# Kernel tuning notes

Measured on AMD Instinct MI355X. Metric: run time of the kernel, lower is better.

## Reference

```python
import jax, jax.numpy as jnp
import numpy as np

N_SEGMENT = 16
N_HEADS = 12
DIM = 768
HEAD_DIM = DIM // N_HEADS
LN_EPS = 1e-5


def setup_inputs() -> dict:
    key = jax.random.key(0)
    ks = jax.random.split(key, 12)
    nt, p, c = 512, 197, DIM
    s = 1.0 / np.sqrt(c)
    return {
        "x": jax.random.normal(ks[0], (nt, p, c), dtype=jnp.float32),
        "w1": jax.random.uniform(ks[1], (1, 1, c), dtype=jnp.float32) * 2.0 - 1.0,
        "ln_g": jnp.ones((c,), dtype=jnp.float32),
        "ln_b": jnp.zeros((c,), dtype=jnp.float32),
        "Wq": jax.random.normal(ks[2], (c, c), dtype=jnp.float32) * s,
        "bq": jax.random.normal(ks[3], (c,), dtype=jnp.float32) * 0.02,
        "Wk": jax.random.normal(ks[4], (c, c), dtype=jnp.float32) * s,
        "bk": jax.random.normal(ks[5], (c,), dtype=jnp.float32) * 0.02,
        "Wv": jax.random.normal(ks[6], (c, c), dtype=jnp.float32) * s,
        "bv": jax.random.normal(ks[7], (c,), dtype=jnp.float32) * 0.02,
        "Wo": jax.random.normal(ks[8], (c, c), dtype=jnp.float32) * s,
        "bo": jax.random.normal(ks[9], (c,), dtype=jnp.float32) * 0.02,
    }


def _layer_norm(x, g, b):
    mu = jnp.mean(x, axis=-1, keepdims=True)
    var = jnp.mean(jnp.square(x - mu), axis=-1, keepdims=True)
    return (x - mu) * jax.lax.rsqrt(var + LN_EPS) * g + b


def _attention(h, Wq, bq, Wk, bk, Wv, bv, Wo, bo):
    # h: [B, T, C]
    B, T, C = h.shape
    def heads(y):
        return y.reshape(B, T, N_HEADS, HEAD_DIM).transpose(0, 2, 1, 3)
    q = heads(h @ Wq + bq)  # [B, H, T, Dh]
    k = heads(h @ Wk + bk)
    v = heads(h @ Wv + bv)
    scores = jnp.einsum("bhtd,bhsd->bhts", q, k) / jnp.sqrt(jnp.float32(HEAD_DIM))
    probs = jax.nn.softmax(scores, axis=-1)
    ctx = jnp.einsum("bhts,bhsd->bhtd", probs, v)
    ctx = ctx.transpose(0, 2, 1, 3).reshape(B, T, C)
    return ctx @ Wo + bo


def reference(x, w1, ln_g, ln_b, Wq, bq, Wk, bk, Wv, bv, Wo, bo):
    nt, p, c = x.shape
    B = nt // N_SEGMENT
    xr = x.reshape(B, N_SEGMENT, p, c)
    s = xr[:, :, 0]  # CLS tokens [B, T, C]
    # weighted temporal shift (in torch this mutates the view; residual sees it)
    s_shift = s.at[:, 1:].add(s[:, :-1] * w1)
    t = _layer_norm(s_shift, ln_g, ln_b)
    t = _attention(t, Wq, bq, Wk, bk, Wv, bv, Wo, bo)
    t = t + s_shift  # residual uses SHIFTED tokens (aliasing in torch source)
    out = xr.at[:, :, 0].set(t)
    return out.reshape(nt, p, c)
```

## Files before the change

### kernel.cpp

```cpp
#include <hip/hip_runtime.h>
#include <math.h>

typedef __attribute__((ext_vector_type(8))) short short8;
typedef __attribute__((ext_vector_type(4))) float f32x4;
typedef __attribute__((ext_vector_type(4))) unsigned short us4;

constexpr int NSEG = 16;
constexpr int CC   = 768;
constexpr int PP   = 197;
constexpr int NH   = 12;
constexpr int HD   = 64;
constexpr int NT   = 512;
constexpr int MN   = NT * CC;
constexpr float LN_EPS = 1e-5f;

constexpr unsigned CPT  = 196 * CC / 4;
constexpr unsigned ROW4 = CC / 4;
constexpr unsigned W4TOT = (unsigned)NT * CPT;

constexpr unsigned L1 = 7077888u;
constexpr unsigned L2 = 5406720u;
constexpr unsigned L3 = 4423680u;
constexpr unsigned L4 = W4TOT - L1 - L2 - L3;
constexpr unsigned B2 = L1, B3 = L1 + L2, B4 = L1 + L2 + L3;

__device__ inline unsigned short f2bf(float f) {
    unsigned u = __float_as_uint(f);
    u += 0x7fffu + ((u >> 16) & 1u);
    return (unsigned short)(u >> 16);
}
__device__ inline float bf2f(unsigned short v) {
    return __uint_as_float((unsigned)v << 16);
}
__device__ inline unsigned cidx(unsigned i) {
    unsigned t = i / CPT;
    return i + t * ROW4 + ROW4;
}
__device__ inline void copy_strided(const float* __restrict__ xf, float* __restrict__ of,
                                    unsigned base, unsigned len,
                                    unsigned ct, unsigned nth) {
    const f32x4* __restrict__ x4 = (const f32x4*)xf;
    f32x4* __restrict__ o4 = (f32x4*)of;
    for (unsigned i = ct; i < len; i += nth) {
        unsigned a = cidx(base + i);
        f32x4 v = __builtin_nontemporal_load(x4 + a);
        o4[a] = v;
    }
}

template<bool ADD_RES, bool BF16_OUT>
__device__ inline void gemm_tile(const unsigned short* __restrict__ A,
                                 const unsigned short* __restrict__ Bt,
                                 const float* __restrict__ bias,
                                 const float* __restrict__ res,
                                 float* __restrict__ outf, unsigned short* __restrict__ outb,
                                 int by, int bx, size_t orow) {
    int tid  = threadIdx.x;
    int lane = tid & 63, wv = tid >> 6;
    int wr = wv >> 1, wc = wv & 1;
    int l15 = lane & 15, lh = lane >> 4;
    int m0 = by * 64 + wr * 32;
    int n0 = bx * 64 + wc * 32;
    f32x4 acc[2][2] = {};
    const unsigned short* Ar0 = A  + (size_t)(m0 + l15) * CC + lh * 8;
    const unsigned short* Ar1 = Ar0 + 16 * CC;
    const unsigned short* Br0 = Bt + (size_t)(n0 + l15) * CC + lh * 8;
    const unsigned short* Br1 = Br0 + 16 * CC;
    #pragma unroll 4
    for (int k0 = 0; k0 < CC; k0 += 32) {
        short8 a0 = *(const short8*)(Ar0 + k0);
        short8 a1 = *(const short8*)(Ar1 + k0);
        short8 b0 = *(const short8*)(Br0 + k0);
        short8 b1 = *(const short8*)(Br1 + k0);
        acc[0][0] = __builtin_amdgcn_mfma_f32_16x16x32_bf16(a0, b0, acc[0][0], 0, 0, 0);
        acc[0][1] = __builtin_amdgcn_mfma_f32_16x16x32_bf16(a0, b1, acc[0][1], 0, 0, 0);
        acc[1][0] = __builtin_amdgcn_mfma_f32_16x16x32_bf16(a1, b0, acc[1][0], 0, 0, 0);
        acc[1][1] = __builtin_amdgcn_mfma_f32_16x16x32_bf16(a1, b1, acc[1][1], 0, 0, 0);
    }
    #pragma unroll
    for (int mf = 0; mf < 2; ++mf)
        #pragma unroll
        for (int nf = 0; nf < 2; ++nf)
            #pragma unroll
            for (int r = 0; r < 4; ++r) {
                int row = m0 + mf * 16 + lh * 4 + r;
                int col = n0 + nf * 16 + l15;
                float v = acc[mf][nf][r] + bias[col];
                if (ADD_RES) v += res[(size_t)row * CC + col];
                if (BF16_OUT) outb[(size_t)row * orow + col] = f2bf(v);
                else          outf[(size_t)row * orow + col] = v;
            }
}

__global__ __launch_bounds__(256) void k1(const float* __restrict__ x, const float* __restrict__ w1,
        const float* __restrict__ g, const float* __restrict__ bln,
        const float* __restrict__ Wq, const float* __restrict__ Wk,
        const float* __restrict__ Wv, const float* __restrict__ Wo,
        float* __restrict__ s_shift, unsigned short* __restrict__ tln,
        unsigned short* __restrict__ wt, float* __restrict__ out) {
    __shared__ float smem[32 * 33];
    int bid = blockIdx.x, tid = threadIdx.x;
    if (bid < 288) {
        #pragma unroll
        for (int rep = 0; rep < 8; ++rep) {
            int idx = bid + rep * 288;
            int mat = idx / 576, tile = idx % 576;
            int tr = tile / 24, tc = tile % 24;
            const float* W = mat == 0 ? Wq : mat == 1 ? Wk : mat == 2 ? Wv : Wo;
            int lr = tid >> 3, lc = (tid & 7) * 4;
            float4 v = *(const float4*)(W + (size_t)(tr * 32 + lr) * CC + tc * 32 + lc);
            smem[lr * 33 + lc + 0] = v.x; smem[lr * 33 + lc + 1] = v.y;
            smem[lr * 33 + lc + 2] = v.z; smem[lr * 33 + lc + 3] = v.w;
            __syncthreads();
            int ln_ = tid >> 3, kc = (tid & 7) * 4;
            us4 o;
            #pragma unroll
            for (int j = 0; j < 4; ++j) o[j] = f2bf(smem[(kc + j) * 33 + ln_]);
            *(us4*)(wt + (size_t)mat * CC * CC + (size_t)(tc * 32 + ln_) * CC + tr * 32 + kc) = o;
            __syncthreads();
        }
    } else if (bid < 288 + NT) {
        int r = bid - 288, seg = r & (NSEG - 1);
        float vals[3]; float local = 0.f;
        #pragma unroll
        for (int i = 0; i < 3; ++i) {
            int c = tid + i * 256;
            float v = x[(size_t)r * PP * CC + c];
            if (seg > 0) v += w1[c] * x[(size_t)(r - 1) * PP * CC + c];
            vals[i] = v; local += v;
        }
        smem[tid] = local; __syncthreads();
        for (int off = 128; off > 0; off >>= 1) {
            if (tid < off) smem[tid] += smem[tid + off];
            __syncthreads();
        }
        float mu = smem[0] * (1.0f / CC); __syncthreads();
        float lv = 0.f;
        #pragma unroll
        for (int i = 0; i < 3; ++i) { float d = vals[i] - mu; lv += d * d; }
        smem[tid] = lv; __syncthreads();
        for (int off = 128; off > 0; off >>= 1) {
            if (tid < off) smem[tid] += smem[tid + off];
            __syncthreads();
        }
        float rstd = rsqrtf(smem[0] * (1.0f / CC) + LN_EPS);
        #pragma unroll
        for (int i = 0; i < 3; ++i) {
            int c = tid + i * 256;
            s_shift[(size_t)r * CC + c] = vals[i];
            tln[(size_t)r * CC + c] = f2bf((vals[i] - mu) * rstd * g[c] + bln[c]);
        }
    }
    copy_strided(x, out, 0u, L1, (unsigned)bid * 256 + tid, 2048u * 256);
}

__global__ __launch_bounds__(256) void k2(const unsigned short* __restrict__ tln,
        const unsigned short* __restrict__ wt,
        const float* __restrict__ bq, const float* __restrict__ bk, const float* __restrict__ bv,
        unsigned short* __restrict__ qkvb,
        const float* __restrict__ x, float* __restrict__ out) {
    int bid = blockIdx.x, tid = threadIdx.x;
    if (bid < 288) {
        int z = bid / 96, rem = bid % 96;
        int by = rem / 12, bx = rem % 12;
        const float* bias = z == 0 ? bq : (z == 1 ? bk : bv);
        gemm_tile<false, true>(tln, wt + (size_t)z * CC * CC, bias, nullptr,
                               nullptr, qkvb + (size_t)z * MN, by, bx, CC);
    } else {
        copy_strided(x, out, B2, L2, (unsigned)(bid - 288) * 256 + tid, 1760u * 256);
    }
}

__global__ __launch_bounds__(256) void k3(const unsigned short* __restrict__ qkvb,
        unsigned short* __restrict__ ctxb,
        const float* __restrict__ x, float* __restrict__ out) {
    int bid = blockIdx.x, tid = threadIdx.x;
    if (bid < 384) {
        const unsigned short* qb = qkvb;
        const unsigned short* kb = qkvb + MN;
        const unsigned short* vb = qkvb + 2 * MN;
        int bb = bid / NH, h = bid % NH;
        __shared__ float qs[16][HD], ks[16][HD], vs[16][HD];
        __shared__ float sc[16][17];
        __shared__ float rsum[16];
        for (int i = tid; i < 16 * HD; i += 256) {
            int t = i >> 6, d = i & 63;
            size_t gidx = (size_t)(bb * NSEG + t) * CC + h * HD + d;
            qs[t][d] = bf2f(qb[gidx]); ks[t][d] = bf2f(kb[gidx]); vs[t][d] = bf2f(vb[gidx]);
        }
        __syncthreads();
        {
            int t = tid >> 4, s = tid & 15;
            float acc = 0.f;
            #pragma unroll
            for (int d = 0; d < HD; ++d) acc += qs[t][d] * ks[s][d];
            sc[t][s] = acc * 0.125f;
        }
        __syncthreads();
        if (tid < 16) {
            float m = -1e30f;
            #pragma unroll
            for (int s = 0; s < 16; ++s) m = fmaxf(m, sc[tid][s]);
            float sum = 0.f;
            #pragma unroll
            for (int s = 0; s < 16; ++s) { float e = __expf(sc[tid][s] - m); sc[tid][s] = e; sum += e; }
            rsum[tid] = sum;
        }
        __syncthreads();
        for (int i = tid; i < 16 * HD; i += 256) {
            int t = i >> 6, d = i & 63;
            float acc = 0.f;
            #pragma unroll
            for (int s = 0; s < 16; ++s) acc += sc[t][s] * vs[s][d];
            ctxb[(size_t)(bb * NSEG + t) * CC + h * HD + d] = f2bf(acc / rsum[t]);
        }
    } else {
        copy_strided(x, out, B3, L3, (unsigned)(bid - 384) * 256 + tid, 1664u * 256);
    }
}

__global__ __launch_bounds__(256) void k4(const unsigned short* __restrict__ ctxb,
        const unsigned short* __restrict__ wto,
        const float* __restrict__ bo, const float* __restrict__ s_shift,
        float* __restrict__ out, const float* __restrict__ x) {
    int bid = blockIdx.x, tid = threadIdx.x;
    if (bid < 96) {
        int by = bid / 12, bx = bid % 12;
        gemm_tile<true, false>(ctxb, wto, bo, s_shift, out, nullptr, by, bx, (size_t)PP * CC);
    } else {
        copy_strided(x, out, B4, L4, (unsigned)(bid - 96) * 256 + tid, 1952u * 256);
    }
}

extern "C" void kernel_launch(void* const* d_in, const int* in_sizes, int n_in,
                              void* d_out, int out_size, void* d_ws, size_t ws_size,
                              hipStream_t stream) {
    const float* x    = (const float*)d_in[0];
    const float* w1   = (const float*)d_in[1];
    const float* ln_g = (const float*)d_in[2];
    const float* ln_b = (const float*)d_in[3];
    const float* Wq   = (const float*)d_in[4];
    const float* bq   = (const float*)d_in[5];
    const float* Wk   = (const float*)d_in[6];
    const float* bk   = (const float*)d_in[7];
    const float* Wv   = (const float*)d_in[8];
    const float* bv   = (const float*)d_in[9];
    const float* Wo   = (const float*)d_in[10];
    const float* bo   = (const float*)d_in[11];
    float* out = (float*)d_out;

    float* s_shift = (float*)d_ws;
    unsigned short* tln  = (unsigned short*)(s_shift + MN);
    unsigned short* qkvb = tln + MN;
    unsigned short* ctxb = qkvb + 3 * (size_t)MN;
    unsigned short* wt   = ctxb + MN;

    k1<<<2048, 256, 0, stream>>>(x, w1, ln_g, ln_b, Wq, Wk, Wv, Wo, s_shift, tln, wt, out);
    k2<<<2048, 256, 0, stream>>>(tln, wt, bq, bk, bv, qkvb, x, out);
    k3<<<2048, 256, 0, stream>>>(qkvb, ctxb, x, out);
    k4<<<2048, 256, 0, stream>>>(ctxb, wt + (size_t)3 * CC * CC, bo, s_shift, out, x);
}
```

Before: 142.2 us.

## Fuse output projection into attention kernel with per-head atomic accumulation

Removes the fourth kernel: each attention block keeps its per-head context in LDS and multiplies it by the matching 64-row slice of Wo with MFMA. It then atomically adds the partial products into the CLS rows of the output. Eight extra blocks in the QKV kernel first write the residual plus bias (s_shift + bo) into those rows, so the atomics accumulate on top of them. This drops one launch and the ctx round-trip through global memory, and the bulk copy is spread across three kernels instead of four. The cost is a 12-way float atomic contention per output element and a non-deterministic summation order.

Result: slower. 153.8 us (+8.2%).

```diff
diff --git a/kernel.cpp b/kernel.cpp
--- a/kernel.cpp
+++ b/kernel.cpp
@@ -18,11 +18,10 @@
 constexpr unsigned ROW4 = CC / 4;
 constexpr unsigned W4TOT = (unsigned)NT * CPT;
 
-constexpr unsigned L1 = 7077888u;
-constexpr unsigned L2 = 5406720u;
-constexpr unsigned L3 = 4423680u;
-constexpr unsigned L4 = W4TOT - L1 - L2 - L3;
-constexpr unsigned B2 = L1, B3 = L1 + L2, B4 = L1 + L2 + L3;
+constexpr unsigned L1 = 7340032u;
+constexpr unsigned L2 = 6291456u;
+constexpr unsigned L3 = W4TOT - L1 - L2;
+constexpr unsigned B2 = L1, B3 = L1 + L2;
 
 __device__ inline unsigned short f2bf(float f) {
     unsigned u = __float_as_uint(f);
@@ -48,13 +47,11 @@
     }
 }
 
-template<bool ADD_RES, bool BF16_OUT>
-__device__ inline void gemm_tile(const unsigned short* __restrict__ A,
-                                 const unsigned short* __restrict__ Bt,
-                                 const float* __restrict__ bias,
-                                 const float* __restrict__ res,
-                                 float* __restrict__ outf, unsigned short* __restrict__ outb,
-                                 int by, int bx, size_t orow) {
+__device__ inline void gemm_tile_qkv(const unsigned short* __restrict__ A,
+                                     const unsigned short* __restrict__ Bt,
+                                     const float* __restrict__ bias,
+                                     unsigned short* __restrict__ outb,
+                                     int by, int bx) {
     int tid  = threadIdx.x;
     int lane = tid & 63, wv = tid >> 6;
     int wr = wv >> 1, wc = wv & 1;
@@ -85,10 +82,7 @@
             for (int r = 0; r < 4; ++r) {
                 int row = m0 + mf * 16 + lh * 4 + r;
                 int col = n0 + nf * 16 + l15;
-                float v = acc[mf][nf][r] + bias[col];
-                if (ADD_RES) v += res[(size_t)row * CC + col];
-                if (BF16_OUT) outb[(size_t)row * orow + col] = f2bf(v);
-                else          outf[(size_t)row * orow + col] = v;
+                outb[(size_t)row * CC + col] = f2bf(acc[mf][nf][r] + bias[col]);
             }
 }
 
@@ -157,6 +151,7 @@
 __global__ __launch_bounds__(256) void k2(const unsigned short* __restrict__ tln,
         const unsigned short* __restrict__ wt,
         const float* __restrict__ bq, const float* __restrict__ bk, const float* __restrict__ bv,
+        const float* __restrict__ bo, const float* __restrict__ s_shift,
         unsigned short* __restrict__ qkvb,
         const float* __restrict__ x, float* __restrict__ out) {
     int bid = blockIdx.x, tid = threadIdx.x;
@@ -164,16 +159,24 @@
         int z = bid / 96, rem = bid % 96;
         int by = rem / 12, bx = rem % 12;
         const float* bias = z == 0 ? bq : (z == 1 ? bk : bv);
-        gemm_tile<false, true>(tln, wt + (size_t)z * CC * CC, bias, nullptr,
-                               nullptr, qkvb + (size_t)z * MN, by, bx, CC);
-    } else {
-        copy_strided(x, out, B2, L2, (unsigned)(bid - 288) * 256 + tid, 1760u * 256);
-    }
+        gemm_tile_qkv(tln, wt + (size_t)z * CC * CC, bias, qkvb + (size_t)z * MN, by, bx);
+        return;
+    }
+    if (bid < 296) {
+        const f32x4* ss4 = (const f32x4*)s_shift;
+        const f32x4* bo4 = (const f32x4*)bo;
+        f32x4* o4 = (f32x4*)out;
+        for (unsigned i = (unsigned)(bid - 288) * 256 + tid; i < (unsigned)NT * ROW4; i += 8u * 256) {
+            unsigned r = i / ROW4, c4 = i % ROW4;
+            o4[(size_t)r * (PP * CC / 4) + c4] = ss4[i] + bo4[c4];
+        }
+    }
+    copy_strided(x, out, B2, L2, (unsigned)(bid - 288) * 256 + tid, 1760u * 256);
 }
 
 __global__ __launch_bounds__(256) void k3(const unsigned short* __restrict__ qkvb,
-        unsigned short* __restrict__ ctxb,
-        const float* __restrict__ x, float* __restrict__ out) {
+        const unsigned short* __restrict__ wto,
+        float* __restrict__ out, const float* __restrict__ x) {
     int bid = blockIdx.x, tid = threadIdx.x;
     if (bid < 384) {
         const unsigned short* qb = qkvb;
@@ -183,6 +186,7 @@
         __shared__ float qs[16][HD], ks[16][HD], vs[16][HD];
         __shared__ float sc[16][17];
         __shared__ float rsum[16];
+        __shared__ unsigned short ctxl[16][72];
         for (int i = tid; i < 16 * HD; i += 256) {
             int t = i >> 6, d = i & 63;
             size_t gidx = (size_t)(bb * NSEG + t) * CC + h * HD + d;
@@ -212,24 +216,29 @@
             float acc = 0.f;
             #pragma unroll
             for (int s = 0; s < 16; ++s) acc += sc[t][s] * vs[s][d];
-            ctxb[(size_t)(bb * NSEG + t) * CC + h * HD + d] = f2bf(acc / rsum[t]);
-        }
-    } else {
-        copy_strided(x, out, B3, L3, (unsigned)(bid - 384) * 256 + tid, 1664u * 256);
-    }
-}
-
-__global__ __launch_bounds__(256) void k4(const unsigned short* __restrict__ ctxb,
-        const unsigned short* __restrict__ wto,
-        const float* __restrict__ bo, const float* __restrict__ s_shift,
-        float* __restrict__ out, const float* __restrict__ x) {
-    int bid = blockIdx.x, tid = threadIdx.x;
-    if (bid < 96) {
-        int by = bid / 12, bx = bid % 12;
-        gemm_tile<true, false>(ctxb, wto, bo, s_shift, out, nullptr, by, bx, (size_t)PP * CC);
-    } else {
-        copy_strided(x, out, B4, L4, (unsigned)(bid - 96) * 256 + tid, 1952u * 256);
-    }
+            ctxl[t][d] = f2bf(acc / rsum[t]);
+        }
+        __syncthreads();
+        int lane = tid & 63, w = tid >> 6;
+        int l15 = lane & 15, lh = lane >> 4;
+        for (int ti = w; ti < 48; ti += 4) {
+            int n0 = ti * 16;
+            f32x4 acc = {0.f, 0.f, 0.f, 0.f};
+            #pragma unroll
+            for (int k0 = 0; k0 < HD; k0 += 32) {
+                short8 a = *(const short8*)&ctxl[l15][k0 + lh * 8];
+                short8 b = *(const short8*)(wto + (size_t)(n0 + l15) * CC + h * HD + k0 + lh * 8);
+                acc = __builtin_amdgcn_mfma_f32_16x16x32_bf16(a, b, acc, 0, 0, 0);
+            }
+            #pragma unroll
+            for (int r = 0; r < 4; ++r) {
+                int row = lh * 4 + r;
+                atomicAdd(&out[(size_t)(bb * NSEG + row) * (size_t)(PP * CC) + n0 + l15], acc[r]);
+            }
+        }
+        return;
+    }
+    copy_strided(x, out, B3, L3, (unsigned)(bid - 384) * 256 + tid, 1664u * 256);
 }
 
 extern "C" void kernel_launch(void* const* d_in, const int* in_sizes, int n_in,
@@ -252,11 +261,9 @@
     float* s_shift = (float*)d_ws;
     unsigned short* tln  = (unsigned short*)(s_shift + MN);
     unsigned short* qkvb = tln + MN;
-    unsigned short* ctxb = qkvb + 3 * (size_t)MN;
-    unsigned short* wt   = ctxb + MN;
+    unsigned short* wt   = qkvb + 3 * (size_t)MN;
 
     k1<<<2048, 256, 0, stream>>>(x, w1, ln_g, ln_b, Wq, Wk, Wv, Wo, s_shift, tln, wt, out);
-    k2<<<2048, 256, 0, stream>>>(tln, wt, bq, bk, bv, qkvb, x, out);
-    k3<<<2048, 256, 0, stream>>>(qkvb, ctxb, x, out);
-    k4<<<2048, 256, 0, stream>>>(ctxb, wt + (size_t)3 * CC * CC, bo, s_shift, out, x);
-}
+    k2<<<2048, 256, 0, stream>>>(tln, wt, bq, bk, bv, bo, s_shift, qkvb, x, out);
+    k3<<<2048, 256, 0, stream>>>(qkvb, wt + (size_t)3 * CC * CC, out, x);
+}
```
